# Performance work log

Hardware: AMD Instinct MI355X
Metric: run time of the kernel (lower is better)

## Reference

```python
import jax, jax.numpy as jnp
import numpy as np

TEMP = 0.07
BASE_TEMP = 0.07
EPS = 1e-8


def setup_inputs() -> dict:
    key = jax.random.key(0)
    features = jax.random.normal(key, (4096, 2, 128), dtype=jnp.float32)
    return {"features": features}


def reference(features):
    B, V, D = features.shape  # bsz, n_views, dim
    # torch.cat(torch.unbind(features, dim=1), dim=0): view-major ordering
    cf = jnp.swapaxes(features, 0, 1).reshape(V * B, D)  # [N, D], N = V*B
    # cosine similarity = normalize rows then GEMM (same math as broadcasted CosineSimilarity)
    n = cf / jnp.maximum(jnp.linalg.norm(cf, axis=-1, keepdims=True), EPS)
    logits = jnp.matmul(n, n.T) / TEMP  # [N, N]
    N = V * B
    logits_mask = 1.0 - jnp.eye(N, dtype=logits.dtype)  # zero out self-contrast
    # SimCLR mask: eye(B) tiled over (anchor_count, contrast_count), minus diagonal
    pos_mask = jnp.tile(jnp.eye(B, dtype=logits.dtype), (V, V)) * logits_mask
    exp_logits = jnp.exp(logits) * logits_mask
    log_prob = logits - jnp.log(exp_logits.sum(axis=1, keepdims=True))
    mean_log_prob_pos = (pos_mask * log_prob).sum(axis=1) / pos_mask.sum(axis=1)
    loss = -(TEMP / BASE_TEMP) * mean_log_prob_pos
    return loss.reshape(V, B).mean()
```

## Files before the change

### kernel.cpp

```cpp
#include <hip/hip_runtime.h>
#include <hip/hip_bf16.h>
#include <math.h>


constexpr int   Bsz   = 4096;
constexpr int   Nrows = 8192;
constexpr int   Dd    = 128;
constexpr float TEMPf = 0.07f;
constexpr float EPSN  = 1e-8f;
constexpr float SCALE = 1.4426950408889634f / 0.07f;
constexpr float LN2   = 0.6931471805599453f;

constexpr int CHUNKS     = 16;
constexpr int CHUNK_COLS = Nrows / CHUNKS;
constexpr int TILE_COLS  = 32;
constexpr int TILES      = CHUNK_COLS / TILE_COLS;

typedef __attribute__((ext_vector_type(8)))  short bf16x8;
typedef __attribute__((ext_vector_type(16))) float floatx16;


__global__ void prep_k(const float* __restrict__ f,
                       __hip_bfloat16* __restrict__ nB,
                       __hip_bfloat16* __restrict__ nA,
                       float* __restrict__ spos) {
    int b    = blockIdx.x * 4 + (threadIdx.x >> 6);
    int lane = threadIdx.x & 63;
    const float* s0 = f + (size_t)(b * 2) * Dd;
    float2 x = *(const float2*)(s0 + lane * 2);
    float2 y = *(const float2*)(s0 + Dd + lane * 2);
    float ss0 = x.x * x.x + x.y * x.y;
    float ss1 = y.x * y.x + y.y * y.y;
    float dt  = x.x * y.x + x.y * y.y;
    #pragma unroll
    for (int off = 32; off; off >>= 1) {
        ss0 += __shfl_xor(ss0, off);
        ss1 += __shfl_xor(ss1, off);
        dt  += __shfl_xor(dt,  off);
    }
    float inv0 = 1.0f / fmaxf(sqrtf(ss0), EPSN);
    float inv1 = 1.0f / fmaxf(sqrtf(ss1), EPSN);
    __hip_bfloat162 h;
    h.x = __float2bfloat16(x.x * inv0);
    h.y = __float2bfloat16(x.y * inv0);
    *(__hip_bfloat162*)(nB + (size_t)b * Dd + lane * 2) = h;
    h.x = __float2bfloat16(x.x * inv0 * SCALE);
    h.y = __float2bfloat16(x.y * inv0 * SCALE);
    *(__hip_bfloat162*)(nA + (size_t)b * Dd + lane * 2) = h;
    h.x = __float2bfloat16(y.x * inv1);
    h.y = __float2bfloat16(y.y * inv1);
    *(__hip_bfloat162*)(nB + (size_t)(Bsz + b) * Dd + lane * 2) = h;
    h.x = __float2bfloat16(y.x * inv1 * SCALE);
    h.y = __float2bfloat16(y.y * inv1 * SCALE);
    *(__hip_bfloat162*)(nA + (size_t)(Bsz + b) * Dd + lane * 2) = h;
    if (lane == 0) spos[b] = dt * inv0 * inv1 / TEMPf;
}

__global__ __launch_bounds__(256, 2)
void main_k(const __hip_bfloat16* __restrict__ nA, const __hip_bfloat16* __restrict__ nB,
            float* __restrict__ partial) {
    __shared__ char lds[TILE_COLS * 256];
    const int tid  = threadIdx.x;
    const int wid  = tid >> 6;
    const int lane = tid & 63;
    const int lo   = lane & 31;
    const int hi   = lane >> 5;
    const int rbase = blockIdx.y * 256 + wid * 64;
    const int cbase = blockIdx.x * CHUNK_COLS;
    const char* abytes = (const char*)nA;
    const char* bbytes = (const char*)nB;

    bf16x8 afrag[2][8];
    #pragma unroll
    for (int s = 0; s < 2; s++) {
        const char* rowp = abytes + (size_t)(rbase + s * 32 + lo) * 256 + hi * 16;
        #pragma unroll
        for (int kc = 0; kc < 8; kc++)
            afrag[s][kc] = *(const bf16x8*)(rowp + kc * 32);
    }

    float sums[2][16];
    #pragma unroll
    for (int s = 0; s < 2; s++)
        #pragma unroll
        for (int r = 0; r < 16; r++) sums[s][r] = 0.f;

    floatx16 zero = {};

    for (int t = 0; t < TILES; t++) {
        const int tc = cbase + t * TILE_COLS;
        __syncthreads();
        {
            int c = tid >> 3, part = tid & 7;
            const char* g = bbytes + (size_t)(tc + c) * 256 + part * 32;
            uint4 g0 = *(const uint4*)g;
            uint4 g1 = *(const uint4*)(g + 16);
            int u0 = part * 2, u1 = u0 + 1;
            *(uint4*)&lds[u0 * 512 + ((c ^ u0) & 31) * 16] = g0;
            *(uint4*)&lds[u1 * 512 + ((c ^ u1) & 31) * 16] = g1;
        }
        __syncthreads();

        floatx16 acc0 = zero, acc1 = zero;
        #pragma unroll
        for (int kc = 0; kc < 8; kc++) {
            int u = kc * 2 + hi;
            bf16x8 bfrag = *(const bf16x8*)&lds[u * 512 + ((lo ^ u) & 31) * 16];
            acc0 = __builtin_amdgcn_mfma_f32_32x32x16_bf16(afrag[0][kc], bfrag, acc0, 0, 0, 0);
            acc1 = __builtin_amdgcn_mfma_f32_32x32x16_bf16(afrag[1][kc], bfrag, acc1, 0, 0, 0);
        }

        #pragma unroll
        for (int s = 0; s < 2; s++) {
            const floatx16& acc = s ? acc1 : acc0;
            bool dtile = (tc == rbase + s * 32);
            #pragma unroll
            for (int r = 0; r < 16; r++) {
                float e = __builtin_amdgcn_exp2f(acc[r]);
                if (dtile && lo == ((r & 3) + 8 * (r >> 2) + 4 * hi)) e = 0.f;
                sums[s][r] += e;
            }
        }
    }

    #pragma unroll
    for (int s = 0; s < 2; s++)
        #pragma unroll
        for (int r = 0; r < 16; r++) {
            float v = sums[s][r];
            #pragma unroll
            for (int off = 1; off < 32; off <<= 1) v += __shfl_xor(v, off);
            sums[s][r] = v;
        }
    if (lo == 0) {
        float* prow = partial + (size_t)blockIdx.x * Nrows;
        #pragma unroll
        for (int s = 0; s < 2; s++)
            #pragma unroll
            for (int r = 0; r < 16; r++) {
                int grow = rbase + s * 32 + (r & 3) + 8 * (r >> 2) + 4 * hi;
                prow[grow] = sums[s][r];
            }
    }
}

__global__ __launch_bounds__(1024)
void final_k(const float* __restrict__ partial, const float* __restrict__ spos,
             float* __restrict__ out) {
    __shared__ float red[16];
    int tid = threadIdx.x;
    float acc = 0.f;
    for (int r = tid; r < Nrows; r += 1024) {
        float se = 0.f;
        #pragma unroll
        for (int c = 0; c < CHUNKS; c++) se += partial[(size_t)c * Nrows + r];
        acc += __builtin_amdgcn_logf(se) * LN2;
    }
    for (int b = tid; b < Bsz; b += 1024) acc -= 2.f * spos[b];
    #pragma unroll
    for (int off = 32; off; off >>= 1) acc += __shfl_xor(acc, off);
    if ((tid & 63) == 0) red[tid >> 6] = acc;
    __syncthreads();
    if (tid == 0) {
        float tt = 0.f;
        for (int w = 0; w < 16; w++) tt += red[w];
        out[0] = tt / (float)Nrows;
    }
}

extern "C" void kernel_launch(void* const* d_in, const int* in_sizes, int n_in,
                              void* d_out, int out_size, void* d_ws, size_t ws_size,
                              hipStream_t stream) {
    const float* f = (const float*)d_in[0];
    char* ws = (char*)d_ws;
    __hip_bfloat16* nB = (__hip_bfloat16*)ws;
    __hip_bfloat16* nA = (__hip_bfloat16*)(ws + (size_t)Nrows * Dd * 2);
    float* partial = (float*)(ws + (size_t)2 * Nrows * Dd * 2);
    float* spos    = (float*)(ws + (size_t)2 * Nrows * Dd * 2
                                 + (size_t)CHUNKS * Nrows * 4);

    prep_k<<<Bsz / 4, 256, 0, stream>>>(f, nB, nA, spos);
    dim3 grid(CHUNKS, Nrows / 256);
    main_k<<<grid, 256, 0, stream>>>(nA, nB, partial);
    final_k<<<1, 1024, 0, stream>>>(partial, spos, (float*)d_out);
}
```

Before: 87.94 us.

## Fuse final reduction into main kernel via atomic last-block counters

New measurement: 127.8 us. 45.3% more time.

```diff
diff --git a/kernel.cpp b/kernel.cpp
--- a/kernel.cpp
+++ b/kernel.cpp
@@ -15,17 +15,30 @@
 constexpr int CHUNK_COLS = Nrows / CHUNKS;
 constexpr int TILE_COLS  = 32;
 constexpr int TILES      = CHUNK_COLS / TILE_COLS;
+constexpr int YGROUPS    = Nrows / 256;
+constexpr int PREPBLKS   = Bsz / 4;
 
 typedef __attribute__((ext_vector_type(8)))  short bf16x8;
 typedef __attribute__((ext_vector_type(16))) float floatx16;
 
+constexpr size_t OFF_NA   = 0x200000;
+constexpr size_t OFF_PART = 0x400000;
+constexpr size_t OFF_SPOS = 0x480000;
+constexpr size_t OFF_YLOG = 0x481000;
+constexpr size_t OFF_CNT  = 0x481080;
 
 __global__ void prep_k(const float* __restrict__ f,
                        __hip_bfloat16* __restrict__ nB,
                        __hip_bfloat16* __restrict__ nA,
-                       float* __restrict__ spos) {
-    int b    = blockIdx.x * 4 + (threadIdx.x >> 6);
-    int lane = threadIdx.x & 63;
+                       float* __restrict__ sposPart,
+                       unsigned int* __restrict__ cnt) {
+    __shared__ float sred[4];
+    int tid  = threadIdx.x;
+    int wid  = tid >> 6;
+    int lane = tid & 63;
+    int b    = blockIdx.x * 4 + wid;
+    if (blockIdx.x == 0 && tid < 33) cnt[tid] = 0;
+
     const float* s0 = f + (size_t)(b * 2) * Dd;
     float2 x = *(const float2*)(s0 + lane * 2);
     float2 y = *(const float2*)(s0 + Dd + lane * 2);
@@ -53,12 +66,17 @@
     h.x = __float2bfloat16(y.x * inv1 * SCALE);
     h.y = __float2bfloat16(y.y * inv1 * SCALE);
     *(__hip_bfloat162*)(nA + (size_t)(Bsz + b) * Dd + lane * 2) = h;
-    if (lane == 0) spos[b] = dt * inv0 * inv1 / TEMPf;
+
+    if (lane == 0) sred[wid] = dt * inv0 * inv1 / TEMPf;
+    __syncthreads();
+    if (tid == 0) sposPart[blockIdx.x] = sred[0] + sred[1] + sred[2] + sred[3];
 }
 
 __global__ __launch_bounds__(256, 2)
 void main_k(const __hip_bfloat16* __restrict__ nA, const __hip_bfloat16* __restrict__ nB,
-            float* __restrict__ partial) {
+            float* __restrict__ partial, const float* __restrict__ sposPart,
+            float* __restrict__ ylog, unsigned int* __restrict__ cnt,
+            float* __restrict__ out) {
     __shared__ char lds[TILE_COLS * 256];
     const int tid  = threadIdx.x;
     const int wid  = tid >> 6;
@@ -142,29 +160,41 @@
                 prow[grow] = sums[s][r];
             }
     }
-}
-
-__global__ __launch_bounds__(1024)
-void final_k(const float* __restrict__ partial, const float* __restrict__ spos,
-             float* __restrict__ out) {
-    __shared__ float red[16];
-    int tid = threadIdx.x;
-    float acc = 0.f;
-    for (int r = tid; r < Nrows; r += 1024) {
+
+    __shared__ int tick, t2s;
+    __shared__ float red[4];
+    __threadfence();
+    if (tid == 0) tick = (int)atomicAdd(&cnt[blockIdx.y], 1u);
+    __syncthreads();
+    if (tick == CHUNKS - 1) {
+        __threadfence();
+        int row = blockIdx.y * 256 + tid;
         float se = 0.f;
         #pragma unroll
-        for (int c = 0; c < CHUNKS; c++) se += partial[(size_t)c * Nrows + r];
-        acc += __builtin_amdgcn_logf(se) * LN2;
-    }
-    for (int b = tid; b < Bsz; b += 1024) acc -= 2.f * spos[b];
-    #pragma unroll
-    for (int off = 32; off; off >>= 1) acc += __shfl_xor(acc, off);
-    if ((tid & 63) == 0) red[tid >> 6] = acc;
-    __syncthreads();
-    if (tid == 0) {
-        float tt = 0.f;
-        for (int w = 0; w < 16; w++) tt += red[w];
-        out[0] = tt / (float)Nrows;
+        for (int c = 0; c < CHUNKS; c++) se += partial[(size_t)c * Nrows + row];
+        float lv = __builtin_amdgcn_logf(se) * LN2;
+        #pragma unroll
+        for (int off = 32; off; off >>= 1) lv += __shfl_xor(lv, off);
+        if (lane == 0) red[wid] = lv;
+        __syncthreads();
+        if (tid == 0) {
+            ylog[blockIdx.y] = red[0] + red[1] + red[2] + red[3];
+            __threadfence();
+            t2s = (int)atomicAdd(&cnt[32], 1u);
+        }
+        __syncthreads();
+        if (t2s == YGROUPS - 1) {
+            __threadfence();
+            float a = 0.f;
+            if (tid < YGROUPS) a += ylog[tid];
+            for (int i = tid; i < PREPBLKS; i += 256) a -= 2.f * sposPart[i];
+            #pragma unroll
+            for (int off = 32; off; off >>= 1) a += __shfl_xor(a, off);
+            if (lane == 0) red[wid] = a;
+            __syncthreads();
+            if (tid == 0)
+                out[0] = (red[0] + red[1] + red[2] + red[3]) / (float)Nrows;
+        }
     }
 }
 
@@ -174,13 +204,14 @@
     const float* f = (const float*)d_in[0];
     char* ws = (char*)d_ws;
     __hip_bfloat16* nB = (__hip_bfloat16*)ws;
-    __hip_bfloat16* nA = (__hip_bfloat16*)(ws + (size_t)Nrows * Dd * 2);
-    float* partial = (float*)(ws + (size_t)2 * Nrows * Dd * 2);
-    float* spos    = (float*)(ws + (size_t)2 * Nrows * Dd * 2
-                                 + (size_t)CHUNKS * Nrows * 4);
-
-    prep_k<<<Bsz / 4, 256, 0, stream>>>(f, nB, nA, spos);
-    dim3 grid(CHUNKS, Nrows / 256);
-    main_k<<<grid, 256, 0, stream>>>(nA, nB, partial);
-    final_k<<<1, 1024, 0, stream>>>(partial, spos, (float*)d_out);
+    __hip_bfloat16* nA = (__hip_bfloat16*)(ws + OFF_NA);
+    float* partial     = (float*)(ws + OFF_PART);
+    float* sposPart    = (float*)(ws + OFF_SPOS);
+    float* ylog        = (float*)(ws + OFF_YLOG);
+    unsigned int* cnt  = (unsigned int*)(ws + OFF_CNT);
+
+    prep_k<<<PREPBLKS, 256, 0, stream>>>(f, nB, nA, sposPart, cnt);
+    dim3 grid(CHUNKS, YGROUPS);
+    main_k<<<grid, 256, 0, stream>>>(nA, nB, partial, sposPart, ylog, cnt,
+                                     (float*)d_out);
 }
```

## Double-buffer LDS column tiles with register prefetch and widen tiles to 64 cols

Applied to the files above, without the earlier changes.

Result: no change. 87.69 us (-0.3%).

```diff
diff --git a/kernel.cpp b/kernel.cpp
--- a/kernel.cpp
+++ b/kernel.cpp
@@ -13,19 +13,29 @@
 
 constexpr int CHUNKS     = 16;
 constexpr int CHUNK_COLS = Nrows / CHUNKS;
-constexpr int TILE_COLS  = 32;
+constexpr int TILE_COLS  = 64;
 constexpr int TILES      = CHUNK_COLS / TILE_COLS;
+constexpr int YGROUPS    = Nrows / 256;
+constexpr int PREPBLKS   = Bsz / 4;
+constexpr int TILE_BYTES = TILE_COLS * 256;
 
 typedef __attribute__((ext_vector_type(8)))  short bf16x8;
 typedef __attribute__((ext_vector_type(16))) float floatx16;
 
+constexpr size_t OFF_NA   = 0x200000;
+constexpr size_t OFF_PART = 0x400000;
+constexpr size_t OFF_SPOS = 0x480000;
 
 __global__ void prep_k(const float* __restrict__ f,
                        __hip_bfloat16* __restrict__ nB,
                        __hip_bfloat16* __restrict__ nA,
-                       float* __restrict__ spos) {
-    int b    = blockIdx.x * 4 + (threadIdx.x >> 6);
-    int lane = threadIdx.x & 63;
+                       float* __restrict__ sposPart) {
+    __shared__ float sred[4];
+    int tid  = threadIdx.x;
+    int wid  = tid >> 6;
+    int lane = tid & 63;
+    int b    = blockIdx.x * 4 + wid;
+
     const float* s0 = f + (size_t)(b * 2) * Dd;
     float2 x = *(const float2*)(s0 + lane * 2);
     float2 y = *(const float2*)(s0 + Dd + lane * 2);
@@ -53,13 +63,16 @@
     h.x = __float2bfloat16(y.x * inv1 * SCALE);
     h.y = __float2bfloat16(y.y * inv1 * SCALE);
     *(__hip_bfloat162*)(nA + (size_t)(Bsz + b) * Dd + lane * 2) = h;
-    if (lane == 0) spos[b] = dt * inv0 * inv1 / TEMPf;
+
+    if (lane == 0) sred[wid] = dt * inv0 * inv1 / TEMPf;
+    __syncthreads();
+    if (tid == 0) sposPart[blockIdx.x] = sred[0] + sred[1] + sred[2] + sred[3];
 }
 
 __global__ __launch_bounds__(256, 2)
 void main_k(const __hip_bfloat16* __restrict__ nA, const __hip_bfloat16* __restrict__ nB,
             float* __restrict__ partial) {
-    __shared__ char lds[TILE_COLS * 256];
+    __shared__ char lds[2][TILE_BYTES];
     const int tid  = threadIdx.x;
     const int wid  = tid >> 6;
     const int lane = tid & 63;
@@ -68,7 +81,13 @@
     const int rbase = blockIdx.y * 256 + wid * 64;
     const int cbase = blockIdx.x * CHUNK_COLS;
     const char* abytes = (const char*)nA;
-    const char* bbytes = (const char*)nB;
+    const char* gb     = (const char*)nB + (size_t)cbase * 256;
+    const int su = tid & 15, scb = tid >> 4;
+
+    uint4 pf[4];
+    #pragma unroll
+    for (int i = 0; i < 4; i++)
+        pf[i] = *(const uint4*)(gb + i * 4096 + tid * 16);
 
     bf16x8 afrag[2][8];
     #pragma unroll
@@ -79,6 +98,13 @@
             afrag[s][kc] = *(const bf16x8*)(rowp + kc * 32);
     }
 
+    #pragma unroll
+    for (int i = 0; i < 4; i++) {
+        int c = i * 16 + scb;
+        *(uint4*)&lds[0][su * 1024 + ((c ^ su) & 63) * 16] = pf[i];
+    }
+    __syncthreads();
+
     float sums[2][16];
     #pragma unroll
     for (int s = 0; s < 2; s++)
@@ -88,39 +114,51 @@
     floatx16 zero = {};
 
     for (int t = 0; t < TILES; t++) {
-        const int tc = cbase + t * TILE_COLS;
-        __syncthreads();
-        {
-            int c = tid >> 3, part = tid & 7;
-            const char* g = bbytes + (size_t)(tc + c) * 256 + part * 32;
-            uint4 g0 = *(const uint4*)g;
-            uint4 g1 = *(const uint4*)(g + 16);
-            int u0 = part * 2, u1 = u0 + 1;
-            *(uint4*)&lds[u0 * 512 + ((c ^ u0) & 31) * 16] = g0;
-            *(uint4*)&lds[u1 * 512 + ((c ^ u1) & 31) * 16] = g1;
-        }
-        __syncthreads();
-
-        floatx16 acc0 = zero, acc1 = zero;
+        if (t + 1 < TILES) {
+            const char* g = gb + (size_t)(t + 1) * TILE_BYTES;
+            #pragma unroll
+            for (int i = 0; i < 4; i++)
+                pf[i] = *(const uint4*)(g + i * 4096 + tid * 16);
+        }
+
+        const char* buf = lds[t & 1];
+        floatx16 acc[2][2];
+        acc[0][0] = zero; acc[0][1] = zero; acc[1][0] = zero; acc[1][1] = zero;
         #pragma unroll
         for (int kc = 0; kc < 8; kc++) {
             int u = kc * 2 + hi;
-            bf16x8 bfrag = *(const bf16x8*)&lds[u * 512 + ((lo ^ u) & 31) * 16];
-            acc0 = __builtin_amdgcn_mfma_f32_32x32x16_bf16(afrag[0][kc], bfrag, acc0, 0, 0, 0);
-            acc1 = __builtin_amdgcn_mfma_f32_32x32x16_bf16(afrag[1][kc], bfrag, acc1, 0, 0, 0);
-        }
-
-        #pragma unroll
-        for (int s = 0; s < 2; s++) {
-            const floatx16& acc = s ? acc1 : acc0;
-            bool dtile = (tc == rbase + s * 32);
-            #pragma unroll
-            for (int r = 0; r < 16; r++) {
-                float e = __builtin_amdgcn_exp2f(acc[r]);
-                if (dtile && lo == ((r & 3) + 8 * (r >> 2) + 4 * hi)) e = 0.f;
-                sums[s][r] += e;
+            int a0 = u * 1024 + ((lo ^ u) & 63) * 16;
+            bf16x8 b0 = *(const bf16x8*)&buf[a0];
+            bf16x8 b1 = *(const bf16x8*)&buf[a0 ^ 512];
+            acc[0][0] = __builtin_amdgcn_mfma_f32_32x32x16_bf16(afrag[0][kc], b0, acc[0][0], 0, 0, 0);
+            acc[1][0] = __builtin_amdgcn_mfma_f32_32x32x16_bf16(afrag[1][kc], b0, acc[1][0], 0, 0, 0);
+            acc[0][1] = __builtin_amdgcn_mfma_f32_32x32x16_bf16(afrag[0][kc], b1, acc[0][1], 0, 0, 0);
+            acc[1][1] = __builtin_amdgcn_mfma_f32_32x32x16_bf16(afrag[1][kc], b1, acc[1][1], 0, 0, 0);
+        }
+
+        bool dtile = (cbase + t * TILE_COLS == rbase);
+        #pragma unroll
+        for (int s = 0; s < 2; s++)
+            #pragma unroll
+            for (int cg = 0; cg < 2; cg++) {
+                #pragma unroll
+                for (int r = 0; r < 16; r++) {
+                    float e = __builtin_amdgcn_exp2f(acc[s][cg][r]);
+                    if (dtile && cg == s && lo == ((r & 3) + 8 * (r >> 2) + 4 * hi))
+                        e = 0.f;
+                    sums[s][r] += e;
+                }
             }
-        }
+
+        if (t + 1 < TILES) {
+            char* wb = lds[(t + 1) & 1];
+            #pragma unroll
+            for (int i = 0; i < 4; i++) {
+                int c = i * 16 + scb;
+                *(uint4*)&wb[su * 1024 + ((c ^ su) & 63) * 16] = pf[i];
+            }
+        }
+        __syncthreads();
     }
 
     #pragma unroll
@@ -145,7 +183,7 @@
 }
 
 __global__ __launch_bounds__(1024)
-void final_k(const float* __restrict__ partial, const float* __restrict__ spos,
+void final_k(const float* __restrict__ partial, const float* __restrict__ sposPart,
              float* __restrict__ out) {
     __shared__ float red[16];
     int tid = threadIdx.x;
@@ -156,7 +194,7 @@
         for (int c = 0; c < CHUNKS; c++) se += partial[(size_t)c * Nrows + r];
         acc += __builtin_amdgcn_logf(se) * LN2;
     }
-    for (int b = tid; b < Bsz; b += 1024) acc -= 2.f * spos[b];
+    for (int i = tid; i < PREPBLKS; i += 1024) acc -= 2.f * sposPart[i];
     #pragma unroll
     for (int off = 32; off; off >>= 1) acc += __shfl_xor(acc, off);
     if ((tid & 63) == 0) red[tid >> 6] = acc;
@@ -174,13 +212,12 @@
     const float* f = (const float*)d_in[0];
     char* ws = (char*)d_ws;
     __hip_bfloat16* nB = (__hip_bfloat16*)ws;
-    __hip_bfloat16* nA = (__hip_bfloat16*)(ws + (size_t)Nrows * Dd * 2);
-    float* partial = (float*)(ws + (size_t)2 * Nrows * Dd * 2);
-    float* spos    = (float*)(ws + (size_t)2 * Nrows * Dd * 2
-                                 + (size_t)CHUNKS * Nrows * 4);
-
-    prep_k<<<Bsz / 4, 256, 0, stream>>>(f, nB, nA, spos);
-    dim3 grid(CHUNKS, Nrows / 256);
+    __hip_bfloat16* nA = (__hip_bfloat16*)(ws + OFF_NA);
+    float* partial     = (float*)(ws + OFF_PART);
+    float* sposPart    = (float*)(ws + OFF_SPOS);
+
+    prep_k<<<PREPBLKS, 256, 0, stream>>>(f, nB, nA, sposPart);
+    dim3 grid(CHUNKS, YGROUPS);
     main_k<<<grid, 256, 0, stream>>>(nA, nB, partial);
-    final_k<<<1, 1024, 0, stream>>>(partial, spos, (float*)d_out);
-}
+    final_k<<<1, 1024, 0, stream>>>(partial, sposPart, (float*)d_out);
+}
```
